# Performance work log

Hardware: AMD Instinct MI355X
Metric: run time of the kernel (lower is better)

## Reference

```python
import jax, jax.numpy as jnp
import numpy as np

B, S, HID, NH = 2, 2048, 1024, 16
HD = HID // NH
SCALE = HD ** -0.5


def elu_plus_one(x):
    return jax.nn.elu(x) + 1.0


def setup_inputs() -> dict:
    key = jax.random.key(0)
    ks = jax.random.split(key, 8)
    w_scale = 0.02  # keep logits in a sane range
    return {
        "hidden_states": jax.random.normal(ks[0], (B, S, HID), jnp.float32),
        "wq": jax.random.normal(ks[1], (HID, HID), jnp.float32) * w_scale,
        "wk": jax.random.normal(ks[2], (HID, HID), jnp.float32) * w_scale,
        "wv": jax.random.normal(ks[3], (HID, HID), jnp.float32) * w_scale,
        "wo": jax.random.normal(ks[4], (HID, HID), jnp.float32) * w_scale,
        "beta": jax.random.normal(ks[5], (NH,), jnp.float32),
        "memory": jax.random.normal(ks[6], (NH, HD, HD), jnp.float32),
        "memory_norm": jax.random.uniform(ks[7], (NH, HD), jnp.float32),
    }


def reference(hidden_states, wq, wk, wv, wo, beta, memory, memory_norm):
    b, s, _ = hidden_states.shape
    # nn.Linear(bias=False): x @ W^T; weights stored [out, in]
    def proj(x, w):
        return jnp.einsum("bsh,oh->bso", x, w).reshape(b, s, NH, HD).transpose(0, 2, 1, 3)

    q = proj(hidden_states, wq)  # [B,H,S,D]
    k = proj(hidden_states, wk)
    v = proj(hidden_states, wv)

    # local causal softmax attention (materializes [B,H,S,S] as the original does)
    scores = jnp.einsum("bhsd,bhtd->bhst", q, k) * SCALE
    causal_mask = jnp.triu(jnp.full((s, s), -jnp.inf, dtype=scores.dtype), k=1)
    attn = jax.nn.softmax(scores + causal_mask, axis=-1)
    a_local = jnp.einsum("bhst,bhtd->bhsd", attn, v)

    # compressive memory retrieval: sigma(Q) @ M / (sigma(Q) @ z)
    sigma_q = elu_plus_one(q)
    a_mem_unnorm = jnp.einsum("bhsd,hde->bhse", sigma_q, memory)
    norm = jnp.clip(jnp.einsum("bhsd,hd->bhs", sigma_q, memory_norm), 1e-6, None)
    a_mem = a_mem_unnorm / norm[..., None]

    gate = jax.nn.sigmoid(beta).reshape(1, NH, 1, 1)
    combined = gate * a_mem + (1.0 - gate) * a_local  # [B,H,S,D]
    combined = combined.transpose(0, 2, 1, 3).reshape(b, s, HID)
    return jnp.einsum("bsh,oh->bso", combined, wo)
```

## Files before the change

### kernel.cpp

```cpp
#include <hip/hip_runtime.h>
#include <stdint.h>

#define LOG2E 1.4426950408889634f

typedef __attribute__((ext_vector_type(8))) __bf16 bf16x8;
typedef __attribute__((ext_vector_type(4))) __bf16 bf16x4;
typedef __attribute__((ext_vector_type(4))) float f32x4;

__device__ inline void gll16(const void* g, void* l) {
  __builtin_amdgcn_global_load_lds(
      (const __attribute__((address_space(1))) void*)g,
      (__attribute__((address_space(3))) void*)l, 16, 0, 0);
}

__global__ __launch_bounds__(256) void cvt_all(
    const float* __restrict__ hs, const float* __restrict__ wq,
    const float* __restrict__ wk, const float* __restrict__ wv,
    const float* __restrict__ wo,
    __bf16* __restrict__ hsb, __bf16* __restrict__ wqb, __bf16* __restrict__ wkb,
    __bf16* __restrict__ wvb, __bf16* __restrict__ wob) {
  int bid = blockIdx.x;
  const float* s; __bf16* d; int i;
  if (bid < 4096) { s = hs; d = hsb; i = bid * 256 + threadIdx.x; }
  else {
    int seg = (bid - 4096) >> 10;
    i = ((bid - 4096) & 1023) * 256 + threadIdx.x;
    s = seg == 0 ? wq : seg == 1 ? wk : seg == 2 ? wv : wo;
    d = seg == 0 ? wqb : seg == 1 ? wkb : seg == 2 ? wvb : wob;
  }
  float4 v = ((const float4*)s)[i];
  bf16x4 o;
  o[0] = (__bf16)v.x; o[1] = (__bf16)v.y; o[2] = (__bf16)v.z; o[3] = (__bf16)v.w;
  *(bf16x4*)&d[(size_t)i * 4] = o;
}

#define KSCALE 0.18033688011112042f
__global__ __launch_bounds__(256, 3) void qkv_gemm(
    const __bf16* __restrict__ hsb, const __bf16* __restrict__ wqb,
    const __bf16* __restrict__ wkb, const __bf16* __restrict__ wvb,
    __bf16* __restrict__ qbuf, __bf16* __restrict__ kbuf,
    __bf16* __restrict__ vtb) {
  constexpr int K = 1024;
  __shared__ __align__(16) __bf16 lta[128 * 32];
  __shared__ __align__(16) __bf16 ltb[128 * 32];
  const int bid = blockIdx.x;
  const int z = bid >> 8, r = bid & 255;
  const __bf16 *A, *Bt;
  int m0, n0;
  if (z < 2) {
    A = hsb; Bt = z ? wkb : wqb;
    m0 = (r & 31) * 128; n0 = (r >> 5) * 128;
  } else {
    A = wvb; Bt = hsb;
    m0 = (r & 7) * 128; n0 = (r >> 3) * 128;
  }
  const int tid = threadIdx.x;
  const int w = tid >> 6, l = tid & 63;
  const int lg = l >> 4, lr = l & 15;
  const int wm = (w >> 1) * 64, wn = (w & 1) * 64;
  f32x4 acc[4][4] = {};
  const int srow = w * 16 + (l >> 2);
  const int scol = (l & 3) * 8;
  const __bf16* ga = A + (size_t)(m0 + srow) * K + scol;
  const __bf16* gb = Bt + (size_t)(n0 + srow) * K + scol;
  __bf16* la = &lta[(size_t)w * 16 * 32];
  __bf16* lb = &ltb[(size_t)w * 16 * 32];
  for (int k0 = 0; k0 < K; k0 += 32) {
    __syncthreads();
    gll16(ga + k0, la);
    gll16(ga + 64 * K + k0, la + 64 * 32);
    gll16(gb + k0, lb);
    gll16(gb + 64 * K + k0, lb + 64 * 32);
    __syncthreads();
    bf16x8 af[4], bfr[4];
#pragma unroll
    for (int i = 0; i < 4; ++i) {
      af[i]  = *(const bf16x8*)&lta[(wm + i * 16 + lr) * 32 + lg * 8];
      bfr[i] = *(const bf16x8*)&ltb[(wn + i * 16 + lr) * 32 + lg * 8];
    }
#pragma unroll
    for (int i = 0; i < 4; ++i)
#pragma unroll
      for (int j = 0; j < 4; ++j)
        acc[i][j] = __builtin_amdgcn_mfma_f32_16x16x32_bf16(af[i], bfr[j], acc[i][j], 0, 0, 0);
  }
#pragma unroll
  for (int i = 0; i < 4; ++i)
#pragma unroll
    for (int j = 0; j < 4; ++j)
#pragma unroll
      for (int rr = 0; rr < 4; ++rr) {
        int gm = m0 + wm + i * 16 + lg * 4 + rr;
        int gn = n0 + wn + j * 16 + lr;
        float v = acc[i][j][rr];
        if (z < 2) {
          int bb = gm >> 11, s = gm & 2047, hh = gn >> 6, d = gn & 63;
          __bf16* dst = z ? kbuf : qbuf;
          if (z) v *= KSCALE;
          dst[(((size_t)bb * 16 + hh) * 2048 + s) * 64 + d] = (__bf16)v;
        } else {
          int bb = gn >> 11, s = gn & 2047, hh = gm >> 6, d = gm & 63;
          vtb[(((size_t)bb * 16 + hh) * 64 + d) * 2048 + s] = (__bf16)v;
        }
      }
}

__global__ __launch_bounds__(256, 2) void gemm_out(const __bf16* __restrict__ A,
                                                   const __bf16* __restrict__ Bt,
                                                   float* __restrict__ C,
                                                   int M, int N) {
  constexpr int K = 1024;
  __shared__ __align__(16) __bf16 lta[128 * 32];
  __shared__ __align__(16) __bf16 ltb[128 * 32];
  const int tid = threadIdx.x;
  const int w = tid >> 6, l = tid & 63;
  const int lg = l >> 4, lr = l & 15;
  const int m0 = blockIdx.x * 128, n0 = blockIdx.y * 128;
  const int wm = (w >> 1) * 64, wn = (w & 1) * 64;
  f32x4 acc[4][4] = {};
  const int srow = w * 16 + (l >> 2);
  const int scol = (l & 3) * 8;
  const __bf16* ga = A + (size_t)(m0 + srow) * K + scol;
  const __bf16* gb = Bt + (size_t)(n0 + srow) * K + scol;
  __bf16* la = &lta[(size_t)w * 16 * 32];
  __bf16* lb = &ltb[(size_t)w * 16 * 32];
  for (int k0 = 0; k0 < K; k0 += 32) {
    __syncthreads();
    gll16(ga + k0, la);
    gll16(ga + 64 * K + k0, la + 64 * 32);
    gll16(gb + k0, lb);
    gll16(gb + 64 * K + k0, lb + 64 * 32);
    __syncthreads();
    bf16x8 af[4], bfr[4];
#pragma unroll
    for (int i = 0; i < 4; ++i) {
      af[i]  = *(const bf16x8*)&lta[(wm + i * 16 + lr) * 32 + lg * 8];
      bfr[i] = *(const bf16x8*)&ltb[(wn + i * 16 + lr) * 32 + lg * 8];
    }
#pragma unroll
    for (int i = 0; i < 4; ++i)
#pragma unroll
      for (int j = 0; j < 4; ++j)
        acc[i][j] = __builtin_amdgcn_mfma_f32_16x16x32_bf16(af[i], bfr[j], acc[i][j], 0, 0, 0);
  }
#pragma unroll
  for (int i = 0; i < 4; ++i)
#pragma unroll
    for (int j = 0; j < 4; ++j)
#pragma unroll
      for (int rr = 0; rr < 4; ++rr) {
        int gm = m0 + wm + i * 16 + lg * 4 + rr;
        int gn = n0 + wn + j * 16 + lr;
        C[(size_t)gm * N + gn] = acc[i][j][rr];
      }
}

#define MTP 72
#define DEFER_THR 11.5f
#define SWZ(row, col) (((row) << 7) + ((col) ^ (((row) & 7) << 3)))
#define SWZK(row, col) (((row) << 6) + ((col) ^ (((row) & 7) << 3)))

__global__ __launch_bounds__(256, 3) void attn_kernel(
    const __bf16* __restrict__ qb,
    const __bf16* __restrict__ kb,
    const __bf16* __restrict__ vtb,
    const float* __restrict__ memory,
    const float* __restrict__ memnorm,
    const float* __restrict__ beta,
    __bf16* __restrict__ comb)
{
  __shared__ __align__(16) __bf16 kt[128 * 64];
  __shared__ __align__(16) __bf16 vt[64 * 128];
  __shared__ __align__(16) __bf16 pt[64 * 128];

  const int tid = threadIdx.x;
  const int w = tid >> 6, l = tid & 63;
  const int lg = l >> 4, lr = l & 15;
  const int bx = blockIdx.x;
  const int t = 31 - (bx >> 5);
  const int bh = bx & 31;
  const int hh = bh & 15, b = bh >> 4;
  const int wq0 = t * 64 + w * 16;
  const int ntiles = (t >> 1) + 1;

  const int s_sk = tid >> 3, s_d8 = (tid & 7) * 8;
  const int s_d = tid >> 4, s_sk8 = (tid & 15) * 8;
  const __bf16* kbase = kb + ((size_t)bh * 2048 + s_sk) * 64 + s_d8;
  const __bf16* vbase = vtb + ((size_t)bh * 64 + s_d) * 2048 + s_sk8;

  bf16x8 qf[2];
#pragma unroll
  for (int kk = 0; kk < 2; ++kk)
    qf[kk] = *(const bf16x8*)(qb + ((size_t)bh * 2048 + wq0 + lr) * 64 + kk * 32 + lg * 8);

  bf16x8 kst[4], vst[4];
#pragma unroll
  for (int is = 0; is < 4; ++is) {
    kst[is] = *(const bf16x8*)(kbase + (size_t)is * 32 * 64);
    vst[is] = *(const bf16x8*)(vbase + is * 16 * 2048);
  }

  float mrun = -1e30f, lsum = 0.f;
  f32x4 apv[4] = {};

  for (int kv = 0; kv < ntiles; ++kv) {
    const int kv0 = kv * 128;
    __syncthreads();
#pragma unroll
    for (int is = 0; is < 4; ++is) {
      *(bf16x8*)&kt[SWZK(s_sk + is * 32, s_d8)] = kst[is];
      *(bf16x8*)&vt[SWZ(s_d + is * 16, s_sk8)] = vst[is];
    }
    __syncthreads();
    if (kv + 1 < ntiles) {
      const size_t off = (size_t)(kv + 1) * 128;
#pragma unroll
      for (int is = 0; is < 4; ++is) {
        kst[is] = *(const bf16x8*)(kbase + ((size_t)is * 32) * 64 + off * 64);
        vst[is] = *(const bf16x8*)(vbase + is * 16 * 2048 + off);
      }
    }

    f32x4 sc[8] = {};
#pragma unroll
    for (int kk = 0; kk < 2; ++kk)
#pragma unroll
      for (int nf = 0; nf < 8; ++nf) {
        bf16x8 kf = *(const bf16x8*)&kt[SWZK(nf * 16 + lr, kk * 32 + lg * 8)];
        sc[nf] = __builtin_amdgcn_mfma_f32_16x16x32_bf16(kf, qf[kk], sc[nf], 0, 0, 0);
      }

    const int qrow = wq0 + lr;
    if (kv0 + 127 > wq0) {
#pragma unroll
      for (int nf = 0; nf < 8; ++nf)
#pragma unroll
        for (int r = 0; r < 4; ++r)
          if (kv0 + nf * 16 + lg * 4 + r > qrow) sc[nf][r] = -1e30f;
    }
    f32x4 m4 = sc[0];
#pragma unroll
    for (int nf = 1; nf < 8; ++nf)
#pragma unroll
      for (int r = 0; r < 4; ++r) m4[r] = fmaxf(m4[r], sc[nf][r]);
    float mx = fmaxf(fmaxf(m4[0], m4[1]), fmaxf(m4[2], m4[3]));
    mx = fmaxf(mx, __shfl_xor(mx, 16, 64));
    mx = fmaxf(mx, __shfl_xor(mx, 32, 64));

    if (!__all(mx - mrun <= DEFER_THR)) {
      float mold = mrun;
      float mn = fmaxf(mold, mx);
      mrun = mn;
      float scl = __builtin_amdgcn_exp2f(mold - mn);
      lsum *= scl;
      float sclq[4];
#pragma unroll
      for (int r = 0; r < 4; ++r) sclq[r] = __shfl(scl, (lg << 2) | r, 16);
#pragma unroll
      for (int nf = 0; nf < 4; ++nf)
#pragma unroll
        for (int r = 0; r < 4; ++r) apv[nf][r] *= sclq[r];
    }

    float rs = 0.f;
#pragma unroll
    for (int nf = 0; nf < 8; ++nf) {
      bf16x4 pk;
#pragma unroll
      for (int r = 0; r < 4; ++r) {
        float pv = __builtin_amdgcn_exp2f(sc[nf][r] - mrun);
        rs += pv;
        pk[r] = (__bf16)pv;
      }
      *(bf16x4*)&pt[SWZ(w * 16 + lr, nf * 16 + lg * 4)] = pk;
    }
    rs += __shfl_xor(rs, 16, 64);
    rs += __shfl_xor(rs, 32, 64);
    lsum += rs;

#pragma unroll
    for (int kk = 0; kk < 4; ++kk) {
      bf16x8 pa = *(const bf16x8*)&pt[SWZ(w * 16 + lr, kk * 32 + lg * 8)];
#pragma unroll
      for (int nf = 0; nf < 4; ++nf) {
        bf16x8 vf = *(const bf16x8*)&vt[SWZ(nf * 16 + lr, kk * 32 + lg * 8)];
        apv[nf] = __builtin_amdgcn_mfma_f32_16x16x32_bf16(pa, vf, apv[nf], 0, 0, 0);
      }
    }
  }

  __syncthreads();
  __bf16* mt = kt;
  for (int i = tid; i < 64 * 64; i += 256) {
    int d = i >> 6, e = i & 63;
    mt[e * MTP + d] = (__bf16)memory[((size_t)hh * 64 + d) * 64 + e];
  }
  for (int i = tid; i < 16 * 64; i += 256) {
    int e = 64 + (i >> 6), d = i & 63;
    mt[e * MTP + d] = (__bf16)memnorm[hh * 64 + d];
  }
  __syncthreads();

  bf16x8 sf[2];
#pragma unroll
  for (int kk = 0; kk < 2; ++kk) {
    bf16x8 q = qf[kk], s;
#pragma unroll
    for (int j = 0; j < 8; ++j) {
      float x = (float)q[j];
      float sg = x > 0.f ? x + 1.f : __builtin_amdgcn_exp2f(x * LOG2E);
      s[j] = (__bf16)sg;
    }
    sf[kk] = s;
  }

  f32x4 am[5] = {};
#pragma unroll
  for (int kk = 0; kk < 2; ++kk)
#pragma unroll
    for (int nf = 0; nf < 5; ++nf) {
      bf16x8 bb = *(const bf16x8*)&mt[(nf * 16 + lr) * MTP + kk * 32 + lg * 8];
      am[nf] = __builtin_amdgcn_mfma_f32_16x16x32_bf16(sf[kk], bb, am[nf], 0, 0, 0);
    }

  const float gate = 1.f / (1.f + __builtin_amdgcn_exp2f(-beta[hh] * LOG2E));
  const float og = 1.f - gate;
  float lsq[4];
#pragma unroll
  for (int r = 0; r < 4; ++r) lsq[r] = __shfl(lsum, (lg << 2) | r, 16);
#pragma unroll
  for (int r = 0; r < 4; ++r) {
    int row = wq0 + lg * 4 + r;
    float linv = __builtin_amdgcn_rcpf(lsq[r]);
    float nrm = fmaxf(am[4][r], 1e-6f);
    float ninv = __builtin_amdgcn_rcpf(nrm);
    size_t base = ((size_t)b * 2048 + row) * 1024 + hh * 64;
#pragma unroll
    for (int nf = 0; nf < 4; ++nf) {
      float al = apv[nf][r] * linv;
      float amv = am[nf][r] * ninv;
      comb[base + nf * 16 + lr] = (__bf16)(gate * amv + og * al);
    }
  }
}

extern "C" void kernel_launch(void* const* d_in, const int* in_sizes, int n_in,
                              void* d_out, int out_size, void* d_ws, size_t ws_size,
                              hipStream_t stream) {
  const float* hs      = (const float*)d_in[0];
  const float* wq      = (const float*)d_in[1];
  const float* wk      = (const float*)d_in[2];
  const float* wv      = (const float*)d_in[3];
  const float* wo      = (const float*)d_in[4];
  const float* beta    = (const float*)d_in[5];
  const float* memory  = (const float*)d_in[6];
  const float* memnorm = (const float*)d_in[7];
  float* out = (float*)d_out;

  char* ws = (char*)d_ws;
  __bf16* hsb  = (__bf16*)(ws);
  __bf16* wqb  = (__bf16*)(ws + ((size_t)8  << 20));
  __bf16* wkb  = (__bf16*)(ws + ((size_t)10 << 20));
  __bf16* wvb  = (__bf16*)(ws + ((size_t)12 << 20));
  __bf16* wob  = (__bf16*)(ws + ((size_t)14 << 20));
  __bf16* qbuf = (__bf16*)(ws + ((size_t)16 << 20));
  __bf16* kbuf = (__bf16*)(ws + ((size_t)24 << 20));
  __bf16* vtb  = (__bf16*)(ws + ((size_t)32 << 20));
  __bf16* comb = (__bf16*)(ws + ((size_t)40 << 20));

  cvt_all<<<8192, 256, 0, stream>>>(hs, wq, wk, wv, wo, hsb, wqb, wkb, wvb, wob);

  qkv_gemm<<<768, 256, 0, stream>>>(hsb, wqb, wkb, wvb, qbuf, kbuf, vtb);

  attn_kernel<<<1024, 256, 0, stream>>>(qbuf, kbuf, vtb, memory, memnorm, beta, comb);

  gemm_out<<<dim3(32, 8), 256, 0, stream>>>(comb, wob, out, 4096, 1024);
}
```

Baseline: 110.3 us.

## Split attention KV range across wave pairs and shrink output GEMM tile

```diff
diff --git a/kernel.cpp b/kernel.cpp
--- a/kernel.cpp
+++ b/kernel.cpp
@@ -111,42 +111,42 @@
                                                    int M, int N) {
   constexpr int K = 1024;
   __shared__ __align__(16) __bf16 lta[128 * 32];
-  __shared__ __align__(16) __bf16 ltb[128 * 32];
+  __shared__ __align__(16) __bf16 ltb[64 * 32];
   const int tid = threadIdx.x;
   const int w = tid >> 6, l = tid & 63;
   const int lg = l >> 4, lr = l & 15;
-  const int m0 = blockIdx.x * 128, n0 = blockIdx.y * 128;
-  const int wm = (w >> 1) * 64, wn = (w & 1) * 64;
-  f32x4 acc[4][4] = {};
-  const int srow = w * 16 + (l >> 2);
-  const int scol = (l & 3) * 8;
+  const int m0 = blockIdx.x * 128, n0 = blockIdx.y * 64;
+  const int wm = (w >> 1) * 64, wn = (w & 1) * 32;
+  f32x4 acc[4][2] = {};
+  const int srow = tid >> 2;
+  const int scol = (tid & 3) * 8;
   const __bf16* ga = A + (size_t)(m0 + srow) * K + scol;
   const __bf16* gb = Bt + (size_t)(n0 + srow) * K + scol;
-  __bf16* la = &lta[(size_t)w * 16 * 32];
-  __bf16* lb = &ltb[(size_t)w * 16 * 32];
+  __bf16* la = &lta[(size_t)w * 512];
+  __bf16* lb = &ltb[(size_t)w * 512];
   for (int k0 = 0; k0 < K; k0 += 32) {
     __syncthreads();
     gll16(ga + k0, la);
-    gll16(ga + 64 * K + k0, la + 64 * 32);
+    gll16(ga + (size_t)64 * K + k0, la + 64 * 32);
     gll16(gb + k0, lb);
-    gll16(gb + 64 * K + k0, lb + 64 * 32);
-    __syncthreads();
-    bf16x8 af[4], bfr[4];
-#pragma unroll
-    for (int i = 0; i < 4; ++i) {
+    __syncthreads();
+    bf16x8 af[4], bfr[2];
+#pragma unroll
+    for (int i = 0; i < 4; ++i)
       af[i]  = *(const bf16x8*)&lta[(wm + i * 16 + lr) * 32 + lg * 8];
-      bfr[i] = *(const bf16x8*)&ltb[(wn + i * 16 + lr) * 32 + lg * 8];
-    }
+#pragma unroll
+    for (int j = 0; j < 2; ++j)
+      bfr[j] = *(const bf16x8*)&ltb[(wn + j * 16 + lr) * 32 + lg * 8];
 #pragma unroll
     for (int i = 0; i < 4; ++i)
 #pragma unroll
-      for (int j = 0; j < 4; ++j)
+      for (int j = 0; j < 2; ++j)
         acc[i][j] = __builtin_amdgcn_mfma_f32_16x16x32_bf16(af[i], bfr[j], acc[i][j], 0, 0, 0);
   }
 #pragma unroll
   for (int i = 0; i < 4; ++i)
 #pragma unroll
-    for (int j = 0; j < 4; ++j)
+    for (int j = 0; j < 2; ++j)
 #pragma unroll
       for (int rr = 0; rr < 4; ++rr) {
         int gm = m0 + wm + i * 16 + lg * 4 + rr;
@@ -155,12 +155,11 @@
       }
 }
 
-#define MTP 72
 #define DEFER_THR 11.5f
 #define SWZ(row, col) (((row) << 7) + ((col) ^ (((row) & 7) << 3)))
 #define SWZK(row, col) (((row) << 6) + ((col) ^ (((row) & 7) << 3)))
 
-__global__ __launch_bounds__(256, 3) void attn_kernel(
+__global__ __launch_bounds__(256, 2) void attn_kernel(
     const __bf16* __restrict__ qb,
     const __bf16* __restrict__ kb,
     const __bf16* __restrict__ vtb,
@@ -169,179 +168,264 @@
     const float* __restrict__ beta,
     __bf16* __restrict__ comb)
 {
-  __shared__ __align__(16) __bf16 kt[128 * 64];
-  __shared__ __align__(16) __bf16 vt[64 * 128];
-  __shared__ __align__(16) __bf16 pt[64 * 128];
+  __shared__ __align__(16) __bf16 kt[2][128 * 64];
+  __shared__ __align__(16) __bf16 vt[2][64 * 128];
+  __shared__ __align__(16) __bf16 pt[4][16 * 128];
 
   const int tid = threadIdx.x;
   const int w = tid >> 6, l = tid & 63;
   const int lg = l >> 4, lr = l & 15;
-  const int bx = blockIdx.x;
-  const int t = 31 - (bx >> 5);
-  const int bh = bx & 31;
+  const int qh = w & 1, par = w >> 1;
+  const int ltid = tid & 127;
+  const int t = 31 - (blockIdx.x >> 5);
+  const int bh = blockIdx.x & 31;
   const int hh = bh & 15, b = bh >> 4;
-  const int wq0 = t * 64 + w * 16;
-  const int ntiles = (t >> 1) + 1;
-
-  const int s_sk = tid >> 3, s_d8 = (tid & 7) * 8;
-  const int s_d = tid >> 4, s_sk8 = (tid & 15) * 8;
-  const __bf16* kbase = kb + ((size_t)bh * 2048 + s_sk) * 64 + s_d8;
-  const __bf16* vbase = vtb + ((size_t)bh * 64 + s_d) * 2048 + s_sk8;
-
-  bf16x8 qf[2];
+  const int wq0 = t * 64 + qh * 32;
+  const int nt = (t >> 1) + 1;
+  const int cA = (nt + 1) >> 1;
+  const int cnt = par ? (nt - cA) : cA;
+  const int kvbase = par ? cA * 128 : 0;
+
+  const int s_sk = ltid >> 3, s_d8 = (ltid & 7) * 8;
+  const int s_d = ltid >> 4, s_sk8 = (ltid & 15) * 8;
+  const __bf16* kbase = kb + ((size_t)bh * 2048 + kvbase + s_sk) * 64 + s_d8;
+  const __bf16* vbase = vtb + ((size_t)bh * 64 + s_d) * 2048 + kvbase + s_sk8;
+
+  bf16x8 qf[2][2];
+#pragma unroll
+  for (int mf = 0; mf < 2; ++mf)
+#pragma unroll
+    for (int kk = 0; kk < 2; ++kk)
+      qf[mf][kk] = *(const bf16x8*)(qb + ((size_t)bh * 2048 + wq0 + mf * 16 + lr) * 64 + kk * 32 + lg * 8);
+
+  bf16x8 kst[8], vst[8];
+  if (cnt > 0) {
+#pragma unroll
+    for (int i = 0; i < 8; ++i) {
+      kst[i] = *(const bf16x8*)(kbase + i * 1024);
+      vst[i] = *(const bf16x8*)(vbase + (size_t)i * 16384);
+    }
+  }
+
+  float mrun[2] = {-1e30f, -1e30f}, lsum[2] = {0.f, 0.f};
+  f32x4 apv[2][4] = {};
+
+  for (int kv = 0; kv < cA; ++kv) {
+    const bool vcur = kv < cnt;
+    __syncthreads();
+    if (vcur) {
+#pragma unroll
+      for (int i = 0; i < 8; ++i) {
+        *(bf16x8*)&kt[par][SWZK(s_sk + i * 16, s_d8)] = kst[i];
+        *(bf16x8*)&vt[par][SWZ(s_d + i * 8, s_sk8)] = vst[i];
+      }
+    }
+    __syncthreads();
+    if (kv + 1 < cnt) {
+#pragma unroll
+      for (int i = 0; i < 8; ++i) {
+        kst[i] = *(const bf16x8*)(kbase + (size_t)(kv + 1) * 8192 + i * 1024);
+        vst[i] = *(const bf16x8*)(vbase + (kv + 1) * 128 + (size_t)i * 16384);
+      }
+    }
+    if (!vcur) continue;
+    const int kv0 = kvbase + kv * 128;
+
+    f32x4 sc[2][8] = {};
+#pragma unroll
+    for (int kk = 0; kk < 2; ++kk)
+#pragma unroll
+      for (int nf = 0; nf < 8; ++nf) {
+        bf16x8 kf = *(const bf16x8*)&kt[par][SWZK(nf * 16 + lr, kk * 32 + lg * 8)];
+#pragma unroll
+        for (int mf = 0; mf < 2; ++mf)
+          sc[mf][nf] = __builtin_amdgcn_mfma_f32_16x16x32_bf16(kf, qf[mf][kk], sc[mf][nf], 0, 0, 0);
+      }
+
+    if (kv0 + 127 > wq0) {
+#pragma unroll
+      for (int mf = 0; mf < 2; ++mf) {
+        const int qrow = wq0 + mf * 16 + lr;
+#pragma unroll
+        for (int nf = 0; nf < 8; ++nf)
+#pragma unroll
+          for (int r = 0; r < 4; ++r)
+            if (kv0 + nf * 16 + lg * 4 + r > qrow) sc[mf][nf][r] = -1e30f;
+      }
+    }
+
+#pragma unroll
+    for (int mf = 0; mf < 2; ++mf) {
+      f32x4 m4 = sc[mf][0];
+#pragma unroll
+      for (int nf = 1; nf < 8; ++nf)
+#pragma unroll
+        for (int r = 0; r < 4; ++r) m4[r] = fmaxf(m4[r], sc[mf][nf][r]);
+      float mx = fmaxf(fmaxf(m4[0], m4[1]), fmaxf(m4[2], m4[3]));
+      mx = fmaxf(mx, __shfl_xor(mx, 16, 64));
+      mx = fmaxf(mx, __shfl_xor(mx, 32, 64));
+      if (!__all(mx - mrun[mf] <= DEFER_THR)) {
+        float mold = mrun[mf];
+        float mn = fmaxf(mold, mx);
+        mrun[mf] = mn;
+        float scl = __builtin_amdgcn_exp2f(mold - mn);
+        lsum[mf] *= scl;
+        float sclq[4];
+#pragma unroll
+        for (int r = 0; r < 4; ++r) sclq[r] = __shfl(scl, (lg << 2) | r, 16);
+#pragma unroll
+        for (int nf = 0; nf < 4; ++nf)
+#pragma unroll
+          for (int r = 0; r < 4; ++r) apv[mf][nf][r] *= sclq[r];
+      }
+    }
+
+    bf16x8 pa0[4];
+    {
+      float rs = 0.f;
+#pragma unroll
+      for (int nf = 0; nf < 8; ++nf) {
+        bf16x4 pk;
+#pragma unroll
+        for (int r = 0; r < 4; ++r) {
+          float pv = __builtin_amdgcn_exp2f(sc[0][nf][r] - mrun[0]);
+          rs += pv;
+          pk[r] = (__bf16)pv;
+        }
+        *(bf16x4*)&pt[w][SWZ(lr, nf * 16 + lg * 4)] = pk;
+      }
+      rs += __shfl_xor(rs, 16, 64);
+      rs += __shfl_xor(rs, 32, 64);
+      lsum[0] += rs;
+#pragma unroll
+      for (int kk = 0; kk < 4; ++kk)
+        pa0[kk] = *(const bf16x8*)&pt[w][SWZ(lr, kk * 32 + lg * 8)];
+    }
+    {
+      float rs = 0.f;
+#pragma unroll
+      for (int nf = 0; nf < 8; ++nf) {
+        bf16x4 pk;
+#pragma unroll
+        for (int r = 0; r < 4; ++r) {
+          float pv = __builtin_amdgcn_exp2f(sc[1][nf][r] - mrun[1]);
+          rs += pv;
+          pk[r] = (__bf16)pv;
+        }
+        *(bf16x4*)&pt[w][SWZ(lr, nf * 16 + lg * 4)] = pk;
+      }
+      rs += __shfl_xor(rs, 16, 64);
+      rs += __shfl_xor(rs, 32, 64);
+      lsum[1] += rs;
+    }
+
+#pragma unroll
+    for (int kk = 0; kk < 4; ++kk) {
+      bf16x8 pa1 = *(const bf16x8*)&pt[w][SWZ(lr, kk * 32 + lg * 8)];
+#pragma unroll
+      for (int nf = 0; nf < 4; ++nf) {
+        bf16x8 vf = *(const bf16x8*)&vt[par][SWZ(nf * 16 + lr, kk * 32 + lg * 8)];
+        apv[0][nf] = __builtin_amdgcn_mfma_f32_16x16x32_bf16(pa0[kk], vf, apv[0][nf], 0, 0, 0);
+        apv[1][nf] = __builtin_amdgcn_mfma_f32_16x16x32_bf16(pa1, vf, apv[1][nf], 0, 0, 0);
+      }
+    }
+  }
+
+  __syncthreads();
+  float* dumpO  = (float*)&kt[0][0];
+  float* dumpML = (float*)&vt[0][0];
+  __bf16* mt = &kt[1][0];
+  if (par == 1) {
+#pragma unroll
+    for (int mf = 0; mf < 2; ++mf) {
+#pragma unroll
+      for (int nf = 0; nf < 4; ++nf)
+#pragma unroll
+        for (int r = 0; r < 4; ++r)
+          dumpO[qh * 2048 + (mf * 16 + lg * 4 + r) * 64 + nf * 16 + lr] = apv[mf][nf][r];
+      dumpML[qh * 64 + mf * 16 + lr] = mrun[mf];
+      dumpML[128 + qh * 64 + mf * 16 + lr] = lsum[mf];
+    }
+  } else {
+    for (int i = tid; i < 64 * 64; i += 128) {
+      int d = i >> 6, e = i & 63;
+      mt[e * 72 + d] = (__bf16)memory[((size_t)hh * 64 + d) * 64 + e];
+    }
+    for (int i = tid; i < 16 * 64; i += 128) {
+      int e = 64 + (i >> 6), d = i & 63;
+      mt[e * 72 + d] = (__bf16)memnorm[hh * 64 + d];
+    }
+  }
+  __syncthreads();
+  if (par == 1) return;
+
+  float lq[2][4], f1v[2], f2v[2];
+#pragma unroll
+  for (int mf = 0; mf < 2; ++mf) {
+    float m2 = dumpML[qh * 64 + mf * 16 + lr];
+    float l2 = dumpML[128 + qh * 64 + mf * 16 + lr];
+    float m1 = mrun[mf];
+    float fm = fmaxf(m1, m2);
+    f1v[mf] = __builtin_amdgcn_exp2f(m1 - fm);
+    f2v[mf] = __builtin_amdgcn_exp2f(m2 - fm);
+    float lm = f1v[mf] * lsum[mf] + f2v[mf] * l2;
+#pragma unroll
+    for (int r = 0; r < 4; ++r) lq[mf][r] = __shfl(lm, (lg << 2) | r, 16);
+  }
+#pragma unroll
+  for (int mf = 0; mf < 2; ++mf)
+#pragma unroll
+    for (int r = 0; r < 4; ++r) {
+      float f1q = __shfl(f1v[mf], (lg << 2) | r, 16);
+      float f2q = __shfl(f2v[mf], (lg << 2) | r, 16);
+#pragma unroll
+      for (int nf = 0; nf < 4; ++nf) {
+        float o2 = dumpO[qh * 2048 + (mf * 16 + lg * 4 + r) * 64 + nf * 16 + lr];
+        apv[mf][nf][r] = f1q * apv[mf][nf][r] + f2q * o2;
+      }
+    }
+
+  bf16x8 sf[2][2];
+#pragma unroll
+  for (int mf = 0; mf < 2; ++mf)
+#pragma unroll
+    for (int kk = 0; kk < 2; ++kk) {
+      bf16x8 q = qf[mf][kk], s;
+#pragma unroll
+      for (int j = 0; j < 8; ++j) {
+        float x = (float)q[j];
+        float sg = x > 0.f ? x + 1.f : __builtin_amdgcn_exp2f(x * LOG2E);
+        s[j] = (__bf16)sg;
+      }
+      sf[mf][kk] = s;
+    }
+  f32x4 am[2][5] = {};
 #pragma unroll
   for (int kk = 0; kk < 2; ++kk)
-    qf[kk] = *(const bf16x8*)(qb + ((size_t)bh * 2048 + wq0 + lr) * 64 + kk * 32 + lg * 8);
-
-  bf16x8 kst[4], vst[4];
-#pragma unroll
-  for (int is = 0; is < 4; ++is) {
-    kst[is] = *(const bf16x8*)(kbase + (size_t)is * 32 * 64);
-    vst[is] = *(const bf16x8*)(vbase + is * 16 * 2048);
-  }
-
-  float mrun = -1e30f, lsum = 0.f;
-  f32x4 apv[4] = {};
-
-  for (int kv = 0; kv < ntiles; ++kv) {
-    const int kv0 = kv * 128;
-    __syncthreads();
-#pragma unroll
-    for (int is = 0; is < 4; ++is) {
-      *(bf16x8*)&kt[SWZK(s_sk + is * 32, s_d8)] = kst[is];
-      *(bf16x8*)&vt[SWZ(s_d + is * 16, s_sk8)] = vst[is];
-    }
-    __syncthreads();
-    if (kv + 1 < ntiles) {
-      const size_t off = (size_t)(kv + 1) * 128;
-#pragma unroll
-      for (int is = 0; is < 4; ++is) {
-        kst[is] = *(const bf16x8*)(kbase + ((size_t)is * 32) * 64 + off * 64);
-        vst[is] = *(const bf16x8*)(vbase + is * 16 * 2048 + off);
-      }
-    }
-
-    f32x4 sc[8] = {};
-#pragma unroll
-    for (int kk = 0; kk < 2; ++kk)
-#pragma unroll
-      for (int nf = 0; nf < 8; ++nf) {
-        bf16x8 kf = *(const bf16x8*)&kt[SWZK(nf * 16 + lr, kk * 32 + lg * 8)];
-        sc[nf] = __builtin_amdgcn_mfma_f32_16x16x32_bf16(kf, qf[kk], sc[nf], 0, 0, 0);
-      }
-
-    const int qrow = wq0 + lr;
-    if (kv0 + 127 > wq0) {
-#pragma unroll
-      for (int nf = 0; nf < 8; ++nf)
-#pragma unroll
-        for (int r = 0; r < 4; ++r)
-          if (kv0 + nf * 16 + lg * 4 + r > qrow) sc[nf][r] = -1e30f;
-    }
-    f32x4 m4 = sc[0];
-#pragma unroll
-    for (int nf = 1; nf < 8; ++nf)
-#pragma unroll
-      for (int r = 0; r < 4; ++r) m4[r] = fmaxf(m4[r], sc[nf][r]);
-    float mx = fmaxf(fmaxf(m4[0], m4[1]), fmaxf(m4[2], m4[3]));
-    mx = fmaxf(mx, __shfl_xor(mx, 16, 64));
-    mx = fmaxf(mx, __shfl_xor(mx, 32, 64));
-
-    if (!__all(mx - mrun <= DEFER_THR)) {
-      float mold = mrun;
-      float mn = fmaxf(mold, mx);
-      mrun = mn;
-      float scl = __builtin_amdgcn_exp2f(mold - mn);
-      lsum *= scl;
-      float sclq[4];
-#pragma unroll
-      for (int r = 0; r < 4; ++r) sclq[r] = __shfl(scl, (lg << 2) | r, 16);
-#pragma unroll
-      for (int nf = 0; nf < 4; ++nf)
-#pragma unroll
-        for (int r = 0; r < 4; ++r) apv[nf][r] *= sclq[r];
-    }
-
-    float rs = 0.f;
-#pragma unroll
-    for (int nf = 0; nf < 8; ++nf) {
-      bf16x4 pk;
-#pragma unroll
-      for (int r = 0; r < 4; ++r) {
-        float pv = __builtin_amdgcn_exp2f(sc[nf][r] - mrun);
-        rs += pv;
-        pk[r] = (__bf16)pv;
-      }
-      *(bf16x4*)&pt[SWZ(w * 16 + lr, nf * 16 + lg * 4)] = pk;
-    }
-    rs += __shfl_xor(rs, 16, 64);
-    rs += __shfl_xor(rs, 32, 64);
-    lsum += rs;
-
-#pragma unroll
-    for (int kk = 0; kk < 4; ++kk) {
-      bf16x8 pa = *(const bf16x8*)&pt[SWZ(w * 16 + lr, kk * 32 + lg * 8)];
-#pragma unroll
-      for (int nf = 0; nf < 4; ++nf) {
-        bf16x8 vf = *(const bf16x8*)&vt[SWZ(nf * 16 + lr, kk * 32 + lg * 8)];
-        apv[nf] = __builtin_amdgcn_mfma_f32_16x16x32_bf16(pa, vf, apv[nf], 0, 0, 0);
-      }
-    }
-  }
-
-  __syncthreads();
-  __bf16* mt = kt;
-  for (int i = tid; i < 64 * 64; i += 256) {
-    int d = i >> 6, e = i & 63;
-    mt[e * MTP + d] = (__bf16)memory[((size_t)hh * 64 + d) * 64 + e];
-  }
-  for (int i = tid; i < 16 * 64; i += 256) {
-    int e = 64 + (i >> 6), d = i & 63;
-    mt[e * MTP + d] = (__bf16)memnorm[hh * 64 + d];
-  }
-  __syncthreads();
-
-  bf16x8 sf[2];
-#pragma unroll
-  for (int kk = 0; kk < 2; ++kk) {
-    bf16x8 q = qf[kk], s;
-#pragma unroll
-    for (int j = 0; j < 8; ++j) {
-      float x = (float)q[j];
-      float sg = x > 0.f ? x + 1.f : __builtin_amdgcn_exp2f(x * LOG2E);
-      s[j] = (__bf16)sg;
-    }
-    sf[kk] = s;
-  }
-
-  f32x4 am[5] = {};
-#pragma unroll
-  for (int kk = 0; kk < 2; ++kk)
 #pragma unroll
     for (int nf = 0; nf < 5; ++nf) {
-      bf16x8 bb = *(const bf16x8*)&mt[(nf * 16 + lr) * MTP + kk * 32 + lg * 8];
-      am[nf] = __builtin_amdgcn_mfma_f32_16x16x32_bf16(sf[kk], bb, am[nf], 0, 0, 0);
+      bf16x8 bb = *(const bf16x8*)&mt[(nf * 16 + lr) * 72 + kk * 32 + lg * 8];
+#pragma unroll
+      for (int mf = 0; mf < 2; ++mf)
+        am[mf][nf] = __builtin_amdgcn_mfma_f32_16x16x32_bf16(sf[mf][kk], bb, am[mf][nf], 0, 0, 0);
     }
 
   const float gate = 1.f / (1.f + __builtin_amdgcn_exp2f(-beta[hh] * LOG2E));
   const float og = 1.f - gate;
-  float lsq[4];
-#pragma unroll
-  for (int r = 0; r < 4; ++r) lsq[r] = __shfl(lsum, (lg << 2) | r, 16);
-#pragma unroll
-  for (int r = 0; r < 4; ++r) {
-    int row = wq0 + lg * 4 + r;
-    float linv = __builtin_amdgcn_rcpf(lsq[r]);
-    float nrm = fmaxf(am[4][r], 1e-6f);
-    float ninv = __builtin_amdgcn_rcpf(nrm);
-    size_t base = ((size_t)b * 2048 + row) * 1024 + hh * 64;
-#pragma unroll
-    for (int nf = 0; nf < 4; ++nf) {
-      float al = apv[nf][r] * linv;
-      float amv = am[nf][r] * ninv;
-      comb[base + nf * 16 + lr] = (__bf16)(gate * amv + og * al);
-    }
-  }
+#pragma unroll
+  for (int mf = 0; mf < 2; ++mf)
+#pragma unroll
+    for (int r = 0; r < 4; ++r) {
+      int row = wq0 + mf * 16 + lg * 4 + r;
+      float linv = __builtin_amdgcn_rcpf(lq[mf][r]);
+      float nrm = fmaxf(am[mf][4][r], 1e-6f);
+      float ninv = __builtin_amdgcn_rcpf(nrm);
+      size_t base = ((size_t)b * 2048 + row) * 1024 + hh * 64;
+#pragma unroll
+      for (int nf = 0; nf < 4; ++nf)
+        comb[base + nf * 16 + lr] =
+            (__bf16)(gate * am[mf][nf][r] * ninv + og * apv[mf][nf][r] * linv);
+    }
 }
 
 extern "C" void kernel_launch(void* const* d_in, const int* in_sizes, int n_in,
@@ -374,5 +458,5 @@
 
   attn_kernel<<<1024, 256, 0, stream>>>(qbuf, kbuf, vtb, memory, memnorm, beta, comb);
 
-  gemm_out<<<dim3(32, 8), 256, 0, stream>>>(comb, wob, out, 4096, 1024);
-}
+  gemm_out<<<dim3(32, 16), 256, 0, stream>>>(comb, wob, out, 4096, 1024);
+}
```

Measured after the change: 114.4 us. 1.04x slower.
